# Optimization experiments

Measured on AMD Instinct MI355X. Metric: run time of the kernel, lower is better.

Reference implementation:

```python
import jax, jax.numpy as jnp
import numpy as np

D = 2048          # input_size
B_NECK = 512      # bottleneck_size
NUM_LANGS = 16
ZETA = 1.1
GAMMA = -0.1
LN_EPS = 1e-5


def setup_inputs() -> dict:
    key = jax.random.key(0)
    ks = jax.random.split(key, 8)
    x = jax.random.normal(ks[0], (8, 2048, D), dtype=jnp.float32)
    # xavier_uniform for linear weights
    lim_d = float(np.sqrt(6.0 / (D + B_NECK)))
    down_w = jax.random.uniform(ks[1], (B_NECK, D), minval=-lim_d, maxval=lim_d, dtype=jnp.float32)
    up_w = jax.random.uniform(ks[2], (D, B_NECK), minval=-lim_d, maxval=lim_d, dtype=jnp.float32)
    down_b = jnp.zeros((B_NECK,), dtype=jnp.float32)
    up_b = jnp.zeros((D,), dtype=jnp.float32)
    ln_g = jnp.ones((D,), dtype=jnp.float32)
    ln_b = jnp.zeros((D,), dtype=jnp.float32)
    down_loga = 0.01 * jax.random.normal(ks[3], (NUM_LANGS, D), dtype=jnp.float32)
    up_loga = 0.01 * jax.random.normal(ks[4], (NUM_LANGS, B_NECK), dtype=jnp.float32)
    return {"x": x, "down_w": down_w, "down_b": down_b, "up_w": up_w,
            "up_b": up_b, "ln_g": ln_g, "ln_b": ln_b,
            "down_loga": down_loga, "up_loga": up_loga, "lang_id": 3}


def _det_mask(loga_row):
    # eval-mode L0 gate: hardtanh(sigmoid(loga)*(zeta-gamma)+gamma, 0, 1)
    return jnp.clip(jax.nn.sigmoid(loga_row) * (ZETA - GAMMA) + GAMMA, 0.0, 1.0)


def reference(x, down_w, down_b, up_w, up_b, ln_g, ln_b, down_loga, up_loga, lang_id):
    shortcut = x
    # LayerNorm over last dim
    mu = jnp.mean(x, axis=-1, keepdims=True)
    var = jnp.mean(jnp.square(x - mu), axis=-1, keepdims=True)
    h = (x - mu) * jax.lax.rsqrt(var + LN_EPS) * ln_g + ln_b
    # down projection with per-input-feature gate (mask scales weight columns)
    dmask = _det_mask(down_loga[lang_id])            # [D]
    h = jnp.einsum('bsd,kd->bsk', h * dmask, down_w) + down_b  # [B,S,B_NECK]
    h = jax.nn.relu(h)
    # up projection with per-bottleneck gate
    umask = _det_mask(up_loga[lang_id])              # [B_NECK]
    h = jnp.einsum('bsk,dk->bsd', h * umask, up_w) + up_b       # [B,S,D]
    return h + shortcut
```

## Files before the change

kernel.cpp:

```cpp
#include <hip/hip_runtime.h>
#include <cstdint>
#include <cstddef>

typedef unsigned short u16;
typedef __attribute__((ext_vector_type(4))) float f32x4;
typedef __attribute__((ext_vector_type(8))) short bf16x8;

#define LN_EPS 1e-5f
#define WAITV(n) asm volatile("s_waitcnt vmcnt(" #n ")" ::: "memory")
#define LGKM0    asm volatile("s_waitcnt lgkmcnt(0)" ::: "memory")
#define BAR()    do { __builtin_amdgcn_s_barrier(); asm volatile("" ::: "memory"); } while (0)

__device__ __forceinline__ u16 f2bf(float f) {
  unsigned int u = __float_as_uint(f);
  u += 0x7FFFu + ((u >> 16) & 1u);
  return (u16)(u >> 16);
}

__device__ __forceinline__ float l0gate(float loga) {
  float s = 1.0f / (1.0f + expf(-loga));
  float v = s * 1.2f - 0.1f;
  return fminf(fmaxf(v, 0.0f), 1.0f);
}

__device__ __forceinline__ void llds16(u16* lds, const u16* g) {
  __builtin_amdgcn_global_load_lds(
      (const __attribute__((address_space(1))) unsigned int*)g,
      (__attribute__((address_space(3))) unsigned int*)lds, 16, 0, 0);
}

__global__ __launch_bounds__(256) void prep_weights(
    const float* __restrict__ dw, const float* __restrict__ uw,
    const float* __restrict__ dloga, const float* __restrict__ uloga,
    const int* __restrict__ lang,
    u16* __restrict__ dwb, u16* __restrict__ uwb) {
  const int lid = lang[0];
  const unsigned i = blockIdx.x * 256u + threadIdx.x;
  dwb[i] = f2bf(dw[i] * l0gate(dloga[lid * 2048 + (i & 2047u)]));
  uwb[i] = f2bf(uw[i] * l0gate(uloga[lid * 512 + (i & 511u)]));
}

__global__ __launch_bounds__(256) void ln_kernel(
    const float* __restrict__ x, const float* __restrict__ g,
    const float* __restrict__ b, u16* __restrict__ h1) {
  const int row = blockIdx.x;
  const int tid = threadIdx.x;
  const float4* xr = (const float4*)(x + (size_t)row * 2048);
  float4 v0 = xr[tid * 2 + 0];
  float4 v1 = xr[tid * 2 + 1];
  float s = v0.x + v0.y + v0.z + v0.w + v1.x + v1.y + v1.z + v1.w;
  float q = v0.x * v0.x + v0.y * v0.y + v0.z * v0.z + v0.w * v0.w +
            v1.x * v1.x + v1.y * v1.y + v1.z * v1.z + v1.w * v1.w;
#pragma unroll
  for (int off = 32; off > 0; off >>= 1) {
    s += __shfl_down(s, off, 64);
    q += __shfl_down(q, off, 64);
  }
  __shared__ float ss[4], sq[4], sstat[2];
  const int wave = tid >> 6, lane = tid & 63;
  if (lane == 0) { ss[wave] = s; sq[wave] = q; }
  __syncthreads();
  if (tid == 0) {
    float S = ss[0] + ss[1] + ss[2] + ss[3];
    float Q = sq[0] + sq[1] + sq[2] + sq[3];
    float mu = S * (1.0f / 2048.0f);
    float var = Q * (1.0f / 2048.0f) - mu * mu;
    sstat[0] = mu;
    sstat[1] = rsqrtf(var + LN_EPS);
  }
  __syncthreads();
  const float mu = sstat[0], rs = sstat[1];
  const float4* g4 = (const float4*)g;
  const float4* b4 = (const float4*)b;
  float4 ga = g4[tid * 2], gb = g4[tid * 2 + 1];
  float4 ba = b4[tid * 2], bb = b4[tid * 2 + 1];
  union { u16 us[8]; uint4 u; } p;
  p.us[0] = f2bf((v0.x - mu) * rs * ga.x + ba.x);
  p.us[1] = f2bf((v0.y - mu) * rs * ga.y + ba.y);
  p.us[2] = f2bf((v0.z - mu) * rs * ga.z + ba.z);
  p.us[3] = f2bf((v0.w - mu) * rs * ga.w + ba.w);
  p.us[4] = f2bf((v1.x - mu) * rs * gb.x + bb.x);
  p.us[5] = f2bf((v1.y - mu) * rs * gb.y + bb.y);
  p.us[6] = f2bf((v1.z - mu) * rs * gb.z + bb.z);
  p.us[7] = f2bf((v1.w - mu) * rs * gb.w + bb.w);
  ((uint4*)(h1 + (size_t)row * 2048))[tid] = p.u;
}

__global__ __launch_bounds__(256) void gemm1(
    const u16* __restrict__ A, const u16* __restrict__ Bw,
    int M, int K, int NX,
    const float* __restrict__ bias,
    u16* __restrict__ outp) {
  const int N = 512;
  __shared__ __align__(16) char smem[65536];
  u16* As = (u16*)smem;
  u16* Bs = (u16*)(smem + 32768);
  float* Cs = (float*)smem;

  const int tid = threadIdx.x;
  const int wave = tid >> 6, lane = tid & 63;
  const int wr = (wave >> 1) * 64, wc = (wave & 1) * 64;
  const int lrow = lane & 15, lk = lane >> 4;

  const int nwg = gridDim.x;
  const int wg = (blockIdx.x & 7) * (nwg >> 3) + (blockIdx.x >> 3);
  const int bx = wg % NX, by = wg / NX;
  const size_t m0 = (size_t)by * 128, n0 = (size_t)bx * 128;

  f32x4 acc[4][4] = {};

  const int srow = lane >> 3;
  const int sslot = ((lane & 7) ^ ((lane >> 3) & 7)) * 8;
  auto STAGE = [&](int buf, int k0) {
#pragma unroll
    for (int c = 0; c < 4; ++c) {
      const int seg = c * 4 + wave;
      const int r = seg * 8 + srow;
      llds16(As + buf * 8192 + seg * 512, A + (m0 + r) * (size_t)K + (k0 + sslot));
      llds16(Bs + buf * 8192 + seg * 512, Bw + (n0 + r) * (size_t)K + (k0 + sslot));
    }
  };

  const int NT = K >> 6;
  STAGE(0, 0);

  for (int t = 0; t < NT; ++t) {
    const int cur = t & 1;
    if (t + 1 < NT) {
      STAGE(cur ^ 1, (t + 1) << 6);
      WAITV(8);
    } else {
      WAITV(0);
    }
    BAR();

    const u16* Ab = As + cur * 8192;
    const u16* Bb = Bs + cur * 8192;
#pragma unroll
    for (int ks = 0; ks < 2; ++ks) {
      bf16x8 af[4], bfr[4];
#pragma unroll
      for (int m = 0; m < 4; ++m)
        af[m] = *(const bf16x8*)&Ab[(wr + m * 16 + lrow) * 64 +
                                    ((unsigned)((ks * 4 + lk) ^ (lane & 7))) * 8];
#pragma unroll
      for (int n = 0; n < 4; ++n)
        bfr[n] = *(const bf16x8*)&Bb[(wc + n * 16 + lrow) * 64 +
                                     ((unsigned)((ks * 4 + lk) ^ (lane & 7))) * 8];
      __builtin_amdgcn_s_setprio(1);
#pragma unroll
      for (int m = 0; m < 4; ++m)
#pragma unroll
        for (int n = 0; n < 4; ++n)
          acc[m][n] = __builtin_amdgcn_mfma_f32_16x16x32_bf16(af[m], bfr[n],
                                                              acc[m][n], 0, 0, 0);
      __builtin_amdgcn_s_setprio(0);
    }
    LGKM0;
    BAR();
  }

#pragma unroll
  for (int n = 0; n < 4; ++n) {
    const int c = wc + n * 16 + lrow;
    const float bv = bias[n0 + c];
#pragma unroll
    for (int m = 0; m < 4; ++m) {
#pragma unroll
      for (int r = 0; r < 4; ++r) {
        const int row = wr + m * 16 + lk * 4 + r;
        Cs[row * 128 + ((c + ((row >> 2) << 3)) & 127)] = acc[m][n][r] + bv;
      }
    }
  }
  LGKM0;
  BAR();

#pragma unroll
  for (int j = 0; j < 8; ++j) {
    const int flat = tid * 8 + j * 2048;
    const int row = flat >> 7, c = flat & 127;
    const int cp = (c + ((row >> 2) << 3)) & 127;
    const f32x4 c0 = *(const f32x4*)&Cs[row * 128 + cp];
    const f32x4 c1 = *(const f32x4*)&Cs[row * 128 + cp + 4];
    union { u16 us[8]; uint4 u; } p;
    p.us[0] = f2bf(fmaxf(c0[0], 0.0f)); p.us[1] = f2bf(fmaxf(c0[1], 0.0f));
    p.us[2] = f2bf(fmaxf(c0[2], 0.0f)); p.us[3] = f2bf(fmaxf(c0[3], 0.0f));
    p.us[4] = f2bf(fmaxf(c1[0], 0.0f)); p.us[5] = f2bf(fmaxf(c1[1], 0.0f));
    p.us[6] = f2bf(fmaxf(c1[2], 0.0f)); p.us[7] = f2bf(fmaxf(c1[3], 0.0f));
    *(uint4*)&outp[(m0 + row) * (size_t)N + n0 + c] = p.u;
  }
}

__global__ __launch_bounds__(256) void gemm2(
    const u16* __restrict__ A, const u16* __restrict__ Bw,
    int M, const float* __restrict__ bias,
    const float* __restrict__ resid, float* __restrict__ outp) {
  const int K = 512, N = 2048;
  __shared__ __align__(16) char smem[65536];
  u16* As = (u16*)smem;
  u16* Bs = (u16*)(smem + 32768);
  float* Cs = (float*)smem;

  const int tid = threadIdx.x;
  const int wave = tid >> 6, lane = tid & 63;
  const int wr = (wave >> 1) * 64, wc = (wave & 1) * 64;
  const int lrow = lane & 15, lk = lane >> 4;

  const int nwg = gridDim.x;
  const int wg = (blockIdx.x & 7) * (nwg >> 3) + (blockIdx.x >> 3);
  const int bx = wg & 15, by = wg >> 4;
  const size_t m0 = (size_t)by * 128, n0 = (size_t)bx * 128;

  f32x4 acc[4][4] = {};

  const int srow = lane >> 3;
  const int sslot = ((lane & 7) ^ ((lane >> 3) & 7)) * 8;
  auto STAGE = [&](int buf, int k0) {
#pragma unroll
    for (int c = 0; c < 4; ++c) {
      const int seg = c * 4 + wave;
      const int r = seg * 8 + srow;
      llds16(As + buf * 8192 + seg * 512, A + (m0 + r) * (size_t)K + (k0 + sslot));
      llds16(Bs + buf * 8192 + seg * 512, Bw + (n0 + r) * (size_t)K + (k0 + sslot));
    }
  };

  f32x4 rsd[16];
  auto RSD = [&](int j) {
    const int flat = tid * 4 + j * 1024;
    const int row = flat >> 7, c = flat & 127;
    rsd[j] = *(const f32x4*)&resid[(m0 + row) * (size_t)N + n0 + c];
  };

  STAGE(0, 0);
#pragma unroll
  for (int t = 0; t < 8; ++t) {
    const int cur = t & 1;
    if (t < 7) {
      STAGE(cur ^ 1, (t + 1) * 64);
      RSD(2 * t); RSD(2 * t + 1);
      WAITV(10);
    } else {
      RSD(14); RSD(15);
      WAITV(4);
    }
    BAR();

    const u16* Ab = As + cur * 8192;
    const u16* Bb = Bs + cur * 8192;
#pragma unroll
    for (int ks = 0; ks < 2; ++ks) {
      bf16x8 af[4], bfr[4];
#pragma unroll
      for (int m = 0; m < 4; ++m)
        af[m] = *(const bf16x8*)&Ab[(wr + m * 16 + lrow) * 64 +
                                    ((unsigned)((ks * 4 + lk) ^ (lane & 7))) * 8];
#pragma unroll
      for (int n = 0; n < 4; ++n)
        bfr[n] = *(const bf16x8*)&Bb[(wc + n * 16 + lrow) * 64 +
                                     ((unsigned)((ks * 4 + lk) ^ (lane & 7))) * 8];
      __builtin_amdgcn_s_setprio(1);
#pragma unroll
      for (int m = 0; m < 4; ++m)
#pragma unroll
        for (int n = 0; n < 4; ++n)
          acc[m][n] = __builtin_amdgcn_mfma_f32_16x16x32_bf16(af[m], bfr[n],
                                                              acc[m][n], 0, 0, 0);
      __builtin_amdgcn_s_setprio(0);
    }
    LGKM0;
    BAR();
  }

#pragma unroll
  for (int n = 0; n < 4; ++n) {
    const int c = wc + n * 16 + lrow;
    const float bv = bias[n0 + c];
#pragma unroll
    for (int m = 0; m < 4; ++m) {
#pragma unroll
      for (int r = 0; r < 4; ++r) {
        const int row = wr + m * 16 + lk * 4 + r;
        Cs[row * 128 + ((c + ((row >> 2) << 3)) & 127)] = acc[m][n][r] + bv;
      }
    }
  }
  LGKM0;
  BAR();

#pragma unroll
  for (int j = 0; j < 16; ++j) {
    const int flat = tid * 4 + j * 1024;
    const int row = flat >> 7, c = flat & 127;
    const f32x4 cc = *(const f32x4*)&Cs[row * 128 + ((c + ((row >> 2) << 3)) & 127)];
    f32x4 o;
    o[0] = cc[0] + rsd[j][0]; o[1] = cc[1] + rsd[j][1];
    o[2] = cc[2] + rsd[j][2]; o[3] = cc[3] + rsd[j][3];
    *(f32x4*)&outp[(m0 + row) * (size_t)N + n0 + c] = o;
  }
}

extern "C" void kernel_launch(void* const* d_in, const int* in_sizes, int n_in,
                              void* d_out, int out_size, void* d_ws, size_t ws_size,
                              hipStream_t stream) {
  const float* x         = (const float*)d_in[0];
  const float* down_w    = (const float*)d_in[1];
  const float* down_b    = (const float*)d_in[2];
  const float* up_w      = (const float*)d_in[3];
  const float* up_b      = (const float*)d_in[4];
  const float* ln_g      = (const float*)d_in[5];
  const float* ln_b      = (const float*)d_in[6];
  const float* down_loga = (const float*)d_in[7];
  const float* up_loga   = (const float*)d_in[8];
  const int*   lang      = (const int*)d_in[9];

  const int D = 2048, BNK = 512;
  const int M = in_sizes[0] / D;
  const int MC = 8192;

  char* ws = (char*)d_ws;
  u16* h1  = (u16*)ws;
  u16* h2  = (u16*)(ws + (size_t)M * D * 2);
  u16* dwb = (u16*)(ws + (size_t)M * D * 2 + (size_t)M * BNK * 2);
  u16* uwb = dwb + (size_t)BNK * D;

  prep_weights<<<(BNK * D) / 256, 256, 0, stream>>>(down_w, up_w, down_loga,
                                                    up_loga, lang, dwb, uwb);

  for (int c = 0; c < M / MC; ++c) {
    const size_t ro = (size_t)c * MC;
    ln_kernel<<<MC, 256, 0, stream>>>(x + ro * D, ln_g, ln_b, h1 + ro * D);
    gemm1<<<(MC / 128) * (BNK / 128), 256, 0, stream>>>(
        h1 + ro * D, dwb, MC, D, BNK / 128, down_b, h2 + ro * BNK);
    gemm2<<<(MC / 128) * (D / 128), 256, 0, stream>>>(
        h2 + ro * BNK, uwb, MC, up_b, x + ro * D, (float*)d_out + ro * D);
  }
}
```

Before: 162.1 us.

## Triple-buffer A tiles with split A/B staging, drop row chunking

Both GEMMs now keep three LDS stages for the A operand and two for B, prefetching A two k-steps ahead so more global loads are in flight per barrier. The vmcnt waits are recomputed to match the new issue order. The host also launches each kernel once over all rows instead of looping over 8192-row chunks. LDS per block grows from 64KB to 80KB, which can lower the number of resident blocks per CU, and the larger single grids change L2 reuse patterns.

```diff
diff --git a/kernel.cpp b/kernel.cpp
--- a/kernel.cpp
+++ b/kernel.cpp
@@ -92,9 +92,8 @@
     const float* __restrict__ bias,
     u16* __restrict__ outp) {
   const int N = 512;
-  __shared__ __align__(16) char smem[65536];
-  u16* As = (u16*)smem;
-  u16* Bs = (u16*)(smem + 32768);
+  __shared__ __align__(16) char smem[81920];
+  u16* Sg = (u16*)smem;
   float* Cs = (float*)smem;
 
   const int tid = threadIdx.x;
@@ -111,31 +110,36 @@
 
   const int srow = lane >> 3;
   const int sslot = ((lane & 7) ^ ((lane >> 3) & 7)) * 8;
-  auto STAGE = [&](int buf, int k0) {
+  auto SA = [&](int buf, int k0) {
 #pragma unroll
     for (int c = 0; c < 4; ++c) {
       const int seg = c * 4 + wave;
-      const int r = seg * 8 + srow;
-      llds16(As + buf * 8192 + seg * 512, A + (m0 + r) * (size_t)K + (k0 + sslot));
-      llds16(Bs + buf * 8192 + seg * 512, Bw + (n0 + r) * (size_t)K + (k0 + sslot));
+      llds16(Sg + buf * 8192 + seg * 512,
+             A + (m0 + seg * 8 + srow) * (size_t)K + (k0 + sslot));
+    }
+  };
+  auto SB = [&](int buf, int k0) {
+#pragma unroll
+    for (int c = 0; c < 4; ++c) {
+      const int seg = c * 4 + wave;
+      llds16(Sg + 24576 + buf * 8192 + seg * 512,
+             Bw + (n0 + seg * 8 + srow) * (size_t)K + (k0 + sslot));
     }
   };
 
   const int NT = K >> 6;
-  STAGE(0, 0);
+  SB(0, 0); SA(0, 0); SA(1, 64);
 
   for (int t = 0; t < NT; ++t) {
-    const int cur = t & 1;
-    if (t + 1 < NT) {
-      STAGE(cur ^ 1, (t + 1) << 6);
-      WAITV(8);
-    } else {
-      WAITV(0);
-    }
+    if (t + 1 < NT) SB((t + 1) & 1, (t + 1) << 6);
+    if (t + 2 < NT) SA((t + 2) % 3, (t + 2) << 6);
+    if (t < NT - 2)       WAITV(12);
+    else if (t == NT - 2) WAITV(8);
+    else                  WAITV(0);
     BAR();
 
-    const u16* Ab = As + cur * 8192;
-    const u16* Bb = Bs + cur * 8192;
+    const u16* Ab = Sg + (t % 3) * 8192;
+    const u16* Bb = Sg + 24576 + (t & 1) * 8192;
 #pragma unroll
     for (int ks = 0; ks < 2; ++ks) {
       bf16x8 af[4], bfr[4];
@@ -197,9 +201,8 @@
     int M, const float* __restrict__ bias,
     const float* __restrict__ resid, float* __restrict__ outp) {
   const int K = 512, N = 2048;
-  __shared__ __align__(16) char smem[65536];
-  u16* As = (u16*)smem;
-  u16* Bs = (u16*)(smem + 32768);
+  __shared__ __align__(16) char smem[81920];
+  u16* Sg = (u16*)smem;
   float* Cs = (float*)smem;
 
   const int tid = threadIdx.x;
@@ -216,13 +219,20 @@
 
   const int srow = lane >> 3;
   const int sslot = ((lane & 7) ^ ((lane >> 3) & 7)) * 8;
-  auto STAGE = [&](int buf, int k0) {
+  auto SA = [&](int buf, int k0) {
 #pragma unroll
     for (int c = 0; c < 4; ++c) {
       const int seg = c * 4 + wave;
-      const int r = seg * 8 + srow;
-      llds16(As + buf * 8192 + seg * 512, A + (m0 + r) * (size_t)K + (k0 + sslot));
-      llds16(Bs + buf * 8192 + seg * 512, Bw + (n0 + r) * (size_t)K + (k0 + sslot));
+      llds16(Sg + buf * 8192 + seg * 512,
+             A + (m0 + seg * 8 + srow) * (size_t)K + (k0 + sslot));
+    }
+  };
+  auto SB = [&](int buf, int k0) {
+#pragma unroll
+    for (int c = 0; c < 4; ++c) {
+      const int seg = c * 4 + wave;
+      llds16(Sg + 24576 + buf * 8192 + seg * 512,
+             Bw + (n0 + seg * 8 + srow) * (size_t)K + (k0 + sslot));
     }
   };
 
@@ -233,22 +243,22 @@
     rsd[j] = *(const f32x4*)&resid[(m0 + row) * (size_t)N + n0 + c];
   };
 
-  STAGE(0, 0);
+  SB(0, 0); SA(0, 0); SA(1, 64);
+
 #pragma unroll
   for (int t = 0; t < 8; ++t) {
-    const int cur = t & 1;
-    if (t < 7) {
-      STAGE(cur ^ 1, (t + 1) * 64);
-      RSD(2 * t); RSD(2 * t + 1);
-      WAITV(10);
-    } else {
-      RSD(14); RSD(15);
-      WAITV(4);
-    }
+    if (t + 1 < 8) SB((t + 1) & 1, (t + 1) * 64);
+    if (t + 2 < 8) SA((t + 2) % 3, (t + 2) * 64);
+    if (t < 7) { RSD(2 * t); RSD(2 * t + 1); }
+    else       { RSD(14); RSD(15); }
+    if (t == 0)      WAITV(14);
+    else if (t <= 5) WAITV(16);
+    else if (t == 6) WAITV(12);
+    else             WAITV(4);
     BAR();
 
-    const u16* Ab = As + cur * 8192;
-    const u16* Bb = Bs + cur * 8192;
+    const u16* Ab = Sg + (t % 3) * 8192;
+    const u16* Bb = Sg + 24576 + (t & 1) * 8192;
 #pragma unroll
     for (int ks = 0; ks < 2; ++ks) {
       bf16x8 af[4], bfr[4];
@@ -317,7 +327,6 @@
 
   const int D = 2048, BNK = 512;
   const int M = in_sizes[0] / D;
-  const int MC = 8192;
 
   char* ws = (char*)d_ws;
   u16* h1  = (u16*)ws;
@@ -327,13 +336,9 @@
 
   prep_weights<<<(BNK * D) / 256, 256, 0, stream>>>(down_w, up_w, down_loga,
                                                     up_loga, lang, dwb, uwb);
-
-  for (int c = 0; c < M / MC; ++c) {
-    const size_t ro = (size_t)c * MC;
-    ln_kernel<<<MC, 256, 0, stream>>>(x + ro * D, ln_g, ln_b, h1 + ro * D);
-    gemm1<<<(MC / 128) * (BNK / 128), 256, 0, stream>>>(
-        h1 + ro * D, dwb, MC, D, BNK / 128, down_b, h2 + ro * BNK);
-    gemm2<<<(MC / 128) * (D / 128), 256, 0, stream>>>(
-        h2 + ro * BNK, uwb, MC, up_b, x + ro * D, (float*)d_out + ro * D);
-  }
-}
+  ln_kernel<<<M, 256, 0, stream>>>(x, ln_g, ln_b, h1);
+  gemm1<<<(M / 128) * (BNK / 128), 256, 0, stream>>>(h1, dwb, M, D, BNK / 128,
+                                                     down_b, h2);
+  gemm2<<<(M / 128) * (D / 128), 256, 0, stream>>>(h2, uwb, M, up_b, x,
+                                                   (float*)d_out);
+}
```

Result: faster. 148.4 us (-8.5%).
